# Performance work log

Measured on AMD Instinct MI355X. Metric: run time of the kernel, lower is better.

Reference implementation:

```python
import jax, jax.numpy as jnp
import numpy as np

B, H, S, D = 4, 16, 2048, 64

def setup_inputs() -> dict:
    key = jax.random.key(0)
    kq, kk, kv = jax.random.split(key, 3)
    q = jax.random.normal(kq, (B, H, S, D), dtype=jnp.float32)
    k = jax.random.normal(kk, (B, H, S, D), dtype=jnp.float32)
    v = jax.random.normal(kv, (B, H, S, D), dtype=jnp.float32)
    # causal mask: True where attention is DISALLOWED (masked_fill semantics)
    row = jnp.arange(S)[:, None]
    col = jnp.arange(S)[None, :]
    attn_mask = (col > row)[None, None, :, :]  # [1,1,S,S] bool
    return {"q": q, "k": k, "v": v, "attn_mask": attn_mask}

def reference(q, k, v, attn_mask):
    scale = 1.0 / jnp.sqrt(jnp.float32(q.shape[-1]))
    # [B,H,S,S] scores
    scores = jnp.einsum("bhqd,bhkd->bhqk", q, k) * scale
    scores = jnp.where(attn_mask, -jnp.inf, scores)
    attn = jax.nn.softmax(scores, axis=-1)
    # dropout p=0 (eval) -> identity
    context = jnp.einsum("bhqk,bhkd->bhqd", attn, v)
    return context
```

## Files before the change

### kernel.cpp

```cpp
#include <hip/hip_runtime.h>

#define BB 4
#define HH 16
#define SS 2048
#define DD 64
#define KST 80

typedef __bf16 bf16x8 __attribute__((ext_vector_type(8)));
typedef __bf16 bf16x2 __attribute__((ext_vector_type(2)));
typedef float  f32x4  __attribute__((ext_vector_type(4)));
typedef unsigned short u16;
typedef unsigned int   u32;

__device__ __forceinline__ u16 f2bf(float f) {
    u32 u = __float_as_uint(f);
    u = (u + 0x7fffu + ((u >> 16) & 1u)) >> 16;
    return (u16)u;
}

__device__ __forceinline__ u32 pack2bf(float a, float b) {
#if __has_builtin(__builtin_amdgcn_cvt_pk_bf16_f32)
    bf16x2 t = __builtin_amdgcn_cvt_pk_bf16_f32(a, b);
    return __builtin_bit_cast(u32, t);
#else
    return (u32)f2bf(a) | ((u32)f2bf(b) << 16);
#endif
}

__global__ void prep(const float* __restrict__ q, const float* __restrict__ k,
                     const float* __restrict__ v,
                     u16* __restrict__ qbf, u16* __restrict__ kbf, u16* __restrict__ vt)
{
    __shared__ u16 tile[64 * 68];
    const int bh = blockIdx.y, s0 = blockIdx.x * 64, tid = threadIdx.x;
    const size_t base = (size_t)bh * SS * DD + (size_t)s0 * DD;
    const float qsc = 0.18033688011112042f;

    {
        const float4* qs4 = (const float4*)(q + base) + tid * 4;
        const float4* ks4 = (const float4*)(k + base) + tid * 4;
        union { u16 h[16]; uint4 u[2]; } oq, ok;
        #pragma unroll
        for (int j = 0; j < 4; ++j) {
            float4 a = qs4[j], b = ks4[j];
            oq.h[j*4+0] = f2bf(a.x * qsc); oq.h[j*4+1] = f2bf(a.y * qsc);
            oq.h[j*4+2] = f2bf(a.z * qsc); oq.h[j*4+3] = f2bf(a.w * qsc);
            ok.h[j*4+0] = f2bf(b.x); ok.h[j*4+1] = f2bf(b.y);
            ok.h[j*4+2] = f2bf(b.z); ok.h[j*4+3] = f2bf(b.w);
        }
        uint4* qd = (uint4*)(qbf + base) + tid * 2;
        uint4* kd = (uint4*)(kbf + base) + tid * 2;
        qd[0] = oq.u[0]; qd[1] = oq.u[1];
        kd[0] = ok.u[0]; kd[1] = ok.u[1];
    }
    {
        const int s4 = (tid >> 4) * 4;
        const int d4 = (tid & 15) * 4;
        float4 r0 = *(const float4*)(v + base + (size_t)(s4 + 0) * DD + d4);
        float4 r1 = *(const float4*)(v + base + (size_t)(s4 + 1) * DD + d4);
        float4 r2 = *(const float4*)(v + base + (size_t)(s4 + 2) * DD + d4);
        float4 r3 = *(const float4*)(v + base + (size_t)(s4 + 3) * DD + d4);
        const float c0[4] = {r0.x, r0.y, r0.z, r0.w};
        const float c1[4] = {r1.x, r1.y, r1.z, r1.w};
        const float c2[4] = {r2.x, r2.y, r2.z, r2.w};
        const float c3[4] = {r3.x, r3.y, r3.z, r3.w};
        #pragma unroll
        for (int i = 0; i < 4; ++i) {
            uint2 o;
            o.x = pack2bf(c0[i], c1[i]);
            o.y = pack2bf(c2[i], c3[i]);
            *(uint2*)(&tile[(d4 + i) * 68 + s4]) = o;
        }
    }
    __syncthreads();
    const int d  = tid >> 2;
    const int ch = tid & 3;
    uint4 o0 = *(const uint4*)(&tile[d * 68 + ch * 16]);
    uint4 o1 = *(const uint4*)(&tile[d * 68 + ch * 16 + 8]);
    u16* dst = vt + (size_t)bh * DD * SS + (size_t)d * SS + s0 + ch * 16;
    *(uint4*)(dst)     = o0;
    *(uint4*)(dst + 8) = o1;
}

__global__ __launch_bounds__(256, 3) void fa3(
    const u16* __restrict__ qbf, const u16* __restrict__ kbf,
    const u16* __restrict__ vtbf, float* __restrict__ out)
{
    const int tid  = threadIdx.x;
    const int lane = tid & 63;
    const int w    = tid >> 6;
    const int quad = lane >> 4;
    const int m16  = lane & 15;
    const int bx   = blockIdx.x;
    const int qblk = 15 - (bx >> 6);
    const int bh   = bx & 63;
    const size_t base  = (size_t)bh * SS * DD;
    const size_t vbase = (size_t)bh * DD * SS;
    const int qw0 = qblk * 128 + w * 32;

    __shared__ __align__(16) u16 Kt[2][64 * KST];
    __shared__ __align__(16) u16 Vt[2][64 * KST];
    __shared__ __align__(16) u16 Pt[4][16 * 64];

    bf16x8 qf[2][2];
    #pragma unroll
    for (int qs = 0; qs < 2; ++qs)
        #pragma unroll
        for (int dc = 0; dc < 2; ++dc)
            qf[qs][dc] = *(const bf16x8*)(qbf + base +
                (size_t)(qw0 + qs * 16 + m16) * DD + dc * 32 + quad * 8);

    const f32x4 vzero = {0.f, 0.f, 0.f, 0.f};
    f32x4 acc[2][4];
    float lrow[2] = {0.f, 0.f};
    #pragma unroll
    for (int qs = 0; qs < 2; ++qs)
        #pragma unroll
        for (int dt = 0; dt < 4; ++dt) acc[qs][dt] = vzero;

    const int ntiles = qblk * 2 + 2;
    const int sr = tid >> 3;
    const int sc = tid & 7;
    const u16* kp = kbf + base + (size_t)sr * DD + sc * 8;
    const u16* vp = vtbf + vbase + (size_t)sr * SS + sc * 8;

    {
        uint4 a0 = *(const uint4*)(kp);
        uint4 a1 = *(const uint4*)(kp + 32 * DD);
        uint4 b0 = *(const uint4*)(vp);
        uint4 b1 = *(const uint4*)(vp + 32 * SS);
        *(uint4*)(&Kt[0][sr * KST + sc * 8])        = a0;
        *(uint4*)(&Kt[0][(sr + 32) * KST + sc * 8]) = a1;
        *(uint4*)(&Vt[0][sr * KST + sc * 8])        = b0;
        *(uint4*)(&Vt[0][(sr + 32) * KST + sc * 8]) = b1;
    }

    for (int t = 0; t < ntiles; ++t) {
        const int kv0 = t * 64;
        const int cur = t & 1, nxt = cur ^ 1;
        __syncthreads();
        const bool haveNext = (t + 1 < ntiles);
        uint4 a0, a1, b0, b1;
        if (haveNext) {
            a0 = *(const uint4*)(kp + (size_t)(kv0 + 64) * DD);
            a1 = *(const uint4*)(kp + (size_t)(kv0 + 96) * DD);
            b0 = *(const uint4*)(vp + kv0 + 64);
            b1 = *(const uint4*)(vp + 32 * SS + kv0 + 64);
        }

        if (kv0 <= qw0 + 31) {
            bf16x8 kf[4][2], vf[4][2];
            #pragma unroll
            for (int st = 0; st < 4; ++st)
                #pragma unroll
                for (int dc = 0; dc < 2; ++dc) {
                    kf[st][dc] = *(const bf16x8*)(&Kt[cur][(st * 16 + m16) * KST + dc * 32 + quad * 8]);
                    vf[st][dc] = *(const bf16x8*)(&Vt[cur][(st * 16 + m16) * KST + dc * 32 + quad * 8]);
                }

            #pragma unroll
            for (int qs = 0; qs < 2; ++qs) {
                const int q0 = qw0 + qs * 16;
                if (kv0 > q0 + 15) continue;
                f32x4 s[4];
                #pragma unroll
                for (int st = 0; st < 4; ++st) {
                    s[st] = vzero;
                    #pragma unroll
                    for (int dc = 0; dc < 2; ++dc)
                        s[st] = __builtin_amdgcn_mfma_f32_16x16x32_bf16(
                            kf[st][dc], qf[qs][dc], s[st], 0, 0, 0);
                }
                if (kv0 + 63 > q0) {
                    const int qq = q0 + m16;
                    #pragma unroll
                    for (int st = 0; st < 4; ++st)
                        #pragma unroll
                        for (int r = 0; r < 4; ++r)
                            if (kv0 + st * 16 + quad * 4 + r > qq) s[st][r] = -1e30f;
                }
                float psum = 0.f;
                u32 pp[4][2];
                #pragma unroll
                for (int st = 0; st < 4; ++st) {
                    #pragma unroll
                    for (int r = 0; r < 4; ++r) {
                        const float p = __builtin_exp2f(s[st][r]);
                        s[st][r] = p;
                        psum += p;
                    }
                    pp[st][0] = pack2bf(s[st][0], s[st][1]);
                    pp[st][1] = pack2bf(s[st][2], s[st][3]);
                }
                lrow[qs] += psum;
                #pragma unroll
                for (int st = 0; st < 4; ++st) {
                    const int Gs = (st * 2 + (quad >> 1)) ^ (m16 & 7);
                    uint2 o; o.x = pp[st][0]; o.y = pp[st][1];
                    *(uint2*)(&Pt[w][m16 * 64 + Gs * 8 + (quad & 1) * 4]) = o;
                }
                #pragma unroll
                for (int kc = 0; kc < 2; ++kc) {
                    const int Gs = (kc * 4 + quad) ^ (m16 & 7);
                    const bf16x8 pf = *(const bf16x8*)(&Pt[w][m16 * 64 + Gs * 8]);
                    #pragma unroll
                    for (int dt = 0; dt < 4; ++dt)
                        acc[qs][dt] = __builtin_amdgcn_mfma_f32_16x16x32_bf16(
                            vf[dt][kc], pf, acc[qs][dt], 0, 0, 0);
                }
            }
        }

        if (haveNext) {
            *(uint4*)(&Kt[nxt][sr * KST + sc * 8])        = a0;
            *(uint4*)(&Kt[nxt][(sr + 32) * KST + sc * 8]) = a1;
            *(uint4*)(&Vt[nxt][sr * KST + sc * 8])        = b0;
            *(uint4*)(&Vt[nxt][(sr + 32) * KST + sc * 8]) = b1;
        }
    }

    #pragma unroll
    for (int qs = 0; qs < 2; ++qs) {
        float l = lrow[qs];
        l += __shfl_xor(l, 16);
        l += __shfl_xor(l, 32);
        const float inv = 1.f / l;
        const int qq = qw0 + qs * 16 + m16;
        #pragma unroll
        for (int dt = 0; dt < 4; ++dt) {
            float4 o = make_float4(acc[qs][dt][0] * inv, acc[qs][dt][1] * inv,
                                   acc[qs][dt][2] * inv, acc[qs][dt][3] * inv);
            *(float4*)(out + base + (size_t)qq * DD + dt * 16 + quad * 4) = o;
        }
    }
}

extern "C" void kernel_launch(void* const* d_in, const int* in_sizes, int n_in,
                              void* d_out, int out_size, void* d_ws, size_t ws_size,
                              hipStream_t stream)
{
    const float* q = (const float*)d_in[0];
    const float* k = (const float*)d_in[1];
    const float* v = (const float*)d_in[2];
    float* out = (float*)d_out;

    const size_t nelem = (size_t)BB * HH * SS * DD;
    u16* qbf  = (u16*)d_ws;
    u16* kbf  = qbf + nelem;
    u16* vtbf = kbf + nelem;

    prep<<<dim3(SS / 64, BB * HH), dim3(256), 0, stream>>>(q, k, v, qbf, kbf, vtbf);
    fa3<<<dim3(16 * 64), dim3(256), 0, stream>>>(qbf, kbf, vtbf, out);
}
```

Measured before the change: 234.6 us.

## Fuse Q conversion into attention kernel, replace P LDS roundtrip with permlane swaps

Q is no longer converted to bf16 in the prep kernel. It is loaded as fp32, scaled and packed into registers directly inside the attention kernel, which removes a global write and read of Q. The P matrix transpose through shared memory is replaced by permlane32/permlane16 swap instructions, which frees LDS and removes the LDS store/load and their latency. Launch bounds rise to 4 blocks per SM, the block-to-q-tile mapping is changed to a serpentine order for causal load balancing, and the row-sum accumulation is split into two partial sums. The risks are the higher occupancy target causing register pressure, and the permlane lane mapping having to match the MFMA operand layout exactly.

```diff
diff --git a/kernel.cpp b/kernel.cpp
--- a/kernel.cpp
+++ b/kernel.cpp
@@ -11,6 +11,7 @@
 typedef float  f32x4  __attribute__((ext_vector_type(4)));
 typedef unsigned short u16;
 typedef unsigned int   u32;
+typedef unsigned int   u32x2 __attribute__((ext_vector_type(2)));
 
 __device__ __forceinline__ u16 f2bf(float f) {
     u32 u = __float_as_uint(f);
@@ -27,30 +28,40 @@
 #endif
 }
 
-__global__ void prep(const float* __restrict__ q, const float* __restrict__ k,
-                     const float* __restrict__ v,
-                     u16* __restrict__ qbf, u16* __restrict__ kbf, u16* __restrict__ vt)
+__device__ __forceinline__ u32x2 pl32(u32 a, u32 b) {
+#if __has_builtin(__builtin_amdgcn_permlane32_swap)
+    return __builtin_amdgcn_permlane32_swap(a, b, false, false);
+#else
+    asm("v_permlane32_swap_b32 %0, %1" : "+v"(a), "+v"(b));
+    u32x2 r; r.x = a; r.y = b; return r;
+#endif
+}
+__device__ __forceinline__ u32x2 pl16(u32 a, u32 b) {
+#if __has_builtin(__builtin_amdgcn_permlane16_swap)
+    return __builtin_amdgcn_permlane16_swap(a, b, false, false);
+#else
+    asm("v_permlane16_swap_b32 %0, %1" : "+v"(a), "+v"(b));
+    u32x2 r; r.x = a; r.y = b; return r;
+#endif
+}
+
+__global__ void prep(const float* __restrict__ k, const float* __restrict__ v,
+                     u16* __restrict__ kbf, u16* __restrict__ vt)
 {
     __shared__ u16 tile[64 * 68];
     const int bh = blockIdx.y, s0 = blockIdx.x * 64, tid = threadIdx.x;
     const size_t base = (size_t)bh * SS * DD + (size_t)s0 * DD;
-    const float qsc = 0.18033688011112042f;
 
     {
-        const float4* qs4 = (const float4*)(q + base) + tid * 4;
         const float4* ks4 = (const float4*)(k + base) + tid * 4;
-        union { u16 h[16]; uint4 u[2]; } oq, ok;
+        union { u16 h[16]; uint4 u[2]; } ok;
         #pragma unroll
         for (int j = 0; j < 4; ++j) {
-            float4 a = qs4[j], b = ks4[j];
-            oq.h[j*4+0] = f2bf(a.x * qsc); oq.h[j*4+1] = f2bf(a.y * qsc);
-            oq.h[j*4+2] = f2bf(a.z * qsc); oq.h[j*4+3] = f2bf(a.w * qsc);
+            float4 b = ks4[j];
             ok.h[j*4+0] = f2bf(b.x); ok.h[j*4+1] = f2bf(b.y);
             ok.h[j*4+2] = f2bf(b.z); ok.h[j*4+3] = f2bf(b.w);
         }
-        uint4* qd = (uint4*)(qbf + base) + tid * 2;
         uint4* kd = (uint4*)(kbf + base) + tid * 2;
-        qd[0] = oq.u[0]; qd[1] = oq.u[1];
         kd[0] = ok.u[0]; kd[1] = ok.u[1];
     }
     {
@@ -82,8 +93,8 @@
     *(uint4*)(dst + 8) = o1;
 }
 
-__global__ __launch_bounds__(256, 3) void fa3(
-    const u16* __restrict__ qbf, const u16* __restrict__ kbf,
+__global__ __launch_bounds__(256, 4) void fa3(
+    const float* __restrict__ q, const u16* __restrict__ kbf,
     const u16* __restrict__ vtbf, float* __restrict__ out)
 {
     const int tid  = threadIdx.x;
@@ -92,23 +103,35 @@
     const int quad = lane >> 4;
     const int m16  = lane & 15;
     const int bx   = blockIdx.x;
-    const int qblk = 15 - (bx >> 6);
-    const int bh   = bx & 63;
+    const int rr   = bx >> 8;
+    const int cc   = bx & 255;
+    const int jj   = cc >> 6;
+    const int bh   = cc & 63;
+    const int qblk = (rr & 1) ? (12 - 4 * rr + jj) : (15 - 4 * rr - jj);
     const size_t base  = (size_t)bh * SS * DD;
     const size_t vbase = (size_t)bh * DD * SS;
     const int qw0 = qblk * 128 + w * 32;
 
     __shared__ __align__(16) u16 Kt[2][64 * KST];
     __shared__ __align__(16) u16 Vt[2][64 * KST];
-    __shared__ __align__(16) u16 Pt[4][16 * 64];
-
+
+    const float qsc = 0.18033688011112042f;
     bf16x8 qf[2][2];
     #pragma unroll
     for (int qs = 0; qs < 2; ++qs)
         #pragma unroll
-        for (int dc = 0; dc < 2; ++dc)
-            qf[qs][dc] = *(const bf16x8*)(qbf + base +
-                (size_t)(qw0 + qs * 16 + m16) * DD + dc * 32 + quad * 8);
+        for (int dc = 0; dc < 2; ++dc) {
+            const float* qp = q + base + (size_t)(qw0 + qs * 16 + m16) * DD
+                              + dc * 32 + quad * 8;
+            float4 a = *(const float4*)(qp);
+            float4 b = *(const float4*)(qp + 4);
+            union { u32 u[4]; bf16x8 v; } t;
+            t.u[0] = pack2bf(a.x * qsc, a.y * qsc);
+            t.u[1] = pack2bf(a.z * qsc, a.w * qsc);
+            t.u[2] = pack2bf(b.x * qsc, b.y * qsc);
+            t.u[3] = pack2bf(b.z * qsc, b.w * qsc);
+            qf[qs][dc] = t.v;
+        }
 
     const f32x4 vzero = {0.f, 0.f, 0.f, 0.f};
     f32x4 acc[2][4];
@@ -165,11 +188,10 @@
                 f32x4 s[4];
                 #pragma unroll
                 for (int st = 0; st < 4; ++st) {
-                    s[st] = vzero;
-                    #pragma unroll
-                    for (int dc = 0; dc < 2; ++dc)
-                        s[st] = __builtin_amdgcn_mfma_f32_16x16x32_bf16(
-                            kf[st][dc], qf[qs][dc], s[st], 0, 0, 0);
+                    s[st] = __builtin_amdgcn_mfma_f32_16x16x32_bf16(
+                        kf[st][0], qf[qs][0], vzero, 0, 0, 0);
+                    s[st] = __builtin_amdgcn_mfma_f32_16x16x32_bf16(
+                        kf[st][1], qf[qs][1], s[st], 0, 0, 0);
                 }
                 if (kv0 + 63 > q0) {
                     const int qq = q0 + m16;
@@ -179,30 +201,29 @@
                         for (int r = 0; r < 4; ++r)
                             if (kv0 + st * 16 + quad * 4 + r > qq) s[st][r] = -1e30f;
                 }
-                float psum = 0.f;
+                float psA = 0.f, psB = 0.f;
                 u32 pp[4][2];
                 #pragma unroll
                 for (int st = 0; st < 4; ++st) {
-                    #pragma unroll
-                    for (int r = 0; r < 4; ++r) {
-                        const float p = __builtin_exp2f(s[st][r]);
-                        s[st][r] = p;
-                        psum += p;
-                    }
-                    pp[st][0] = pack2bf(s[st][0], s[st][1]);
-                    pp[st][1] = pack2bf(s[st][2], s[st][3]);
-                }
-                lrow[qs] += psum;
-                #pragma unroll
-                for (int st = 0; st < 4; ++st) {
-                    const int Gs = (st * 2 + (quad >> 1)) ^ (m16 & 7);
-                    uint2 o; o.x = pp[st][0]; o.y = pp[st][1];
-                    *(uint2*)(&Pt[w][m16 * 64 + Gs * 8 + (quad & 1) * 4]) = o;
-                }
+                    const float p0 = __builtin_exp2f(s[st][0]);
+                    const float p1 = __builtin_exp2f(s[st][1]);
+                    const float p2 = __builtin_exp2f(s[st][2]);
+                    const float p3 = __builtin_exp2f(s[st][3]);
+                    psA += p0; psB += p1; psA += p2; psB += p3;
+                    pp[st][0] = pack2bf(p0, p1);
+                    pp[st][1] = pack2bf(p2, p3);
+                }
+                lrow[qs] += psA + psB;
                 #pragma unroll
                 for (int kc = 0; kc < 2; ++kc) {
-                    const int Gs = (kc * 4 + quad) ^ (m16 & 7);
-                    const bf16x8 pf = *(const bf16x8*)(&Pt[w][m16 * 64 + Gs * 8]);
+                    u32x2 t0 = pl32(pp[2 * kc][0], pp[2 * kc + 1][0]);
+                    u32x2 r0 = pl16(t0.x, t0.y);
+                    u32x2 t1 = pl32(pp[2 * kc][1], pp[2 * kc + 1][1]);
+                    u32x2 r1 = pl16(t1.x, t1.y);
+                    union { u32 u[4]; bf16x8 v; } pfu;
+                    pfu.u[0] = r0.x; pfu.u[1] = r1.x;
+                    pfu.u[2] = r0.y; pfu.u[3] = r1.y;
+                    const bf16x8 pf = pfu.v;
                     #pragma unroll
                     for (int dt = 0; dt < 4; ++dt)
                         acc[qs][dt] = __builtin_amdgcn_mfma_f32_16x16x32_bf16(
@@ -245,10 +266,9 @@
     float* out = (float*)d_out;
 
     const size_t nelem = (size_t)BB * HH * SS * DD;
-    u16* qbf  = (u16*)d_ws;
-    u16* kbf  = qbf + nelem;
+    u16* kbf  = (u16*)d_ws;
     u16* vtbf = kbf + nelem;
 
-    prep<<<dim3(SS / 64, BB * HH), dim3(256), 0, stream>>>(q, k, v, qbf, kbf, vtbf);
-    fa3<<<dim3(16 * 64), dim3(256), 0, stream>>>(qbf, kbf, vtbf, out);
-}
+    prep<<<dim3(SS / 64, BB * HH), dim3(256), 0, stream>>>(k, v, kbf, vtbf);
+    fa3<<<dim3(16 * 64), dim3(256), 0, stream>>>(q, kbf, vtbf, out);
+}
```

Measured after the change: 338.5 us. 1.44x slower.
